# Optimization experiments

Hardware: AMD Instinct MI355X
Metric: run time of the kernel (lower is better)

The kernel has to match this reference:

```python
import jax, jax.numpy as jnp
import numpy as np

B, S, D, H = 4, 2048, 1024, 16
HD = D // H  # head_dim = 64


def setup_inputs() -> dict:
    key = jax.random.key(0)
    ks = jax.random.split(key, 5)
    hidden_states = jax.random.normal(ks[0], (B, S, D), dtype=jnp.float32)
    # GPT-2 Conv1D: out = x @ W + b, W shape [in, out]
    w_attn = jax.random.normal(ks[1], (D, 3 * D), dtype=jnp.float32) * 0.02
    b_attn = jnp.zeros((3 * D,), dtype=jnp.float32)
    w_proj = jax.random.normal(ks[2], (D, D), dtype=jnp.float32) * 0.02
    b_proj = jnp.zeros((D,), dtype=jnp.float32)
    return {"hidden_states": hidden_states, "w_attn": w_attn, "b_attn": b_attn,
            "w_proj": w_proj, "b_proj": b_proj}


def reference(hidden_states, w_attn, b_attn, w_proj, b_proj):
    b, s, d = hidden_states.shape
    qkv = hidden_states @ w_attn + b_attn                     # [B,S,3D]
    q, k, v = jnp.split(qkv, 3, axis=-1)
    # split heads -> [B,H,S,HD]
    def heads(x):
        return x.reshape(b, s, H, HD).transpose(0, 2, 1, 3)
    q, k, v = heads(q), heads(k), heads(v)
    # scaled dot product; GPT-2 divides by sqrt(head_dim)
    scores = jnp.einsum("bhqd,bhkd->bhqk", q, k) / jnp.sqrt(jnp.float32(HD))
    causal = jnp.tril(jnp.ones((s, s), dtype=bool))           # [S,S]
    neg = jnp.finfo(scores.dtype).min
    scores = jnp.where(causal[None, None, :, :], scores, neg)
    attn = jax.nn.softmax(scores, axis=-1)
    ctx = jnp.einsum("bhqk,bhkd->bhqd", attn, v)              # [B,H,S,HD]
    ctx = ctx.transpose(0, 2, 1, 3).reshape(b, s, d)          # merge heads
    return ctx @ w_proj + b_proj
```

## Files before the change

kernel.cpp:

```cpp
#include <hip/hip_runtime.h>
#include <hip/hip_bf16.h>

typedef __bf16 bf16;
typedef bf16 bf16x8 __attribute__((ext_vector_type(8)));
typedef bf16 bf16x4 __attribute__((ext_vector_type(4)));
typedef float f32x4 __attribute__((ext_vector_type(4)));
typedef float f32x16 __attribute__((ext_vector_type(16)));
typedef unsigned int uint2v __attribute__((ext_vector_type(2)));

#define MFMA16(a, b, c) __builtin_amdgcn_mfma_f32_16x16x32_bf16(a, b, c, 0, 0, 0)
#define MFMA32(a, b, c) __builtin_amdgcn_mfma_f32_32x32x16_bf16(a, b, c, 0, 0, 0)

constexpr int Bn = 4, Sn = 2048, Dn = 1024, Hn = 16, HDn = 64;
constexpr int Mn = Bn * Sn;

__device__ __forceinline__ bf16x8 cvt8(float4 a, float4 b) {
  bf16x8 v = {(bf16)a.x, (bf16)a.y, (bf16)a.z, (bf16)a.w,
              (bf16)b.x, (bf16)b.y, (bf16)b.z, (bf16)b.w};
  return v;
}

__device__ __forceinline__ void load_lds16(const bf16* g, bf16* l) {
  __builtin_amdgcn_global_load_lds(
      (const __attribute__((address_space(1))) void*)g,
      (__attribute__((address_space(3))) void*)l, 16, 0, 0);
}

__device__ __forceinline__ unsigned cvt_pk_bf16(float lo, float hi) {
  unsigned r;
  asm("v_cvt_pk_bf16_f32 %0, %1, %2" : "=v"(r) : "v"(lo), "v"(hi));
  return r;
}

__global__ __launch_bounds__(256) void k_cvt(const float* __restrict__ in,
                                             bf16* __restrict__ out) {
  int i = blockIdx.x * 256 + threadIdx.x;
  const float4* p = (const float4*)in + (size_t)i * 2;
  float4 a = p[0], b = p[1];
  *((bf16x8*)out + i) = cvt8(a, b);
}

__global__ __launch_bounds__(256) void k_transpose_cvt(const float* __restrict__ in,
                                                       bf16* __restrict__ out,
                                                       int K, int N) {
  __shared__ alignas(16) bf16 t[64][72];
  const int n0 = blockIdx.x * 64, k0 = blockIdx.y * 64;
  const int tid = threadIdx.x;
  {
    int row = tid >> 2;
    int c16 = (tid & 3) * 16;
    const float* src = in + (size_t)(k0 + row) * N + n0 + c16;
    float4 f0 = ((const float4*)src)[0];
    float4 f1 = ((const float4*)src)[1];
    float4 f2 = ((const float4*)src)[2];
    float4 f3 = ((const float4*)src)[3];
    *(bf16x8*)&t[row][c16] = cvt8(f0, f1);
    *(bf16x8*)&t[row][c16 + 8] = cvt8(f2, f3);
  }
  __syncthreads();
#pragma unroll
  for (int i = 0; i < 2; i++) {
    int c = tid + i * 256;
    int nrow = c >> 3, kcol8 = (c & 7) * 8;
    bf16x8 v;
#pragma unroll
    for (int j = 0; j < 8; j++) v[j] = t[kcol8 + j][nrow];
    *(bf16x8*)(out + (size_t)(n0 + nrow) * K + k0 + kcol8) = v;
  }
}


__global__ __launch_bounds__(256) void k_gemm_qkv(const bf16* __restrict__ A,
                                                  const bf16* __restrict__ BT,
                                                  const float* __restrict__ bias,
                                                  bf16* __restrict__ Qo,
                                                  bf16* __restrict__ Ko,
                                                  bf16* __restrict__ Vt) {
  __shared__ alignas(16) bf16 la[128 * 32];
  __shared__ alignas(16) bf16 lb[128 * 32];
  const int tid = threadIdx.x;
  const int w = tid >> 6, lane = tid & 63, l15 = lane & 15, quad = lane >> 4;
  const int wm = w >> 1, wn = w & 1;
  const int m0 = blockIdx.y * 128, n0 = blockIdx.x * 128;
  const int lrow = lane >> 2, lcol = (lane & 3) * 8;

  f32x4 acc[4][4];
#pragma unroll
  for (int i = 0; i < 4; i++)
#pragma unroll
    for (int j = 0; j < 4; j++) acc[i][j] = f32x4{0.f, 0.f, 0.f, 0.f};

  for (int k0 = 0; k0 < 1024; k0 += 32) {
    __syncthreads();
    load_lds16(A + (size_t)(m0 + w * 16 + lrow) * 1024 + k0 + lcol, &la[w * 512]);
    load_lds16(A + (size_t)(m0 + 64 + w * 16 + lrow) * 1024 + k0 + lcol, &la[(w + 4) * 512]);
    load_lds16(BT + (size_t)(n0 + w * 16 + lrow) * 1024 + k0 + lcol, &lb[w * 512]);
    load_lds16(BT + (size_t)(n0 + 64 + w * 16 + lrow) * 1024 + k0 + lcol, &lb[(w + 4) * 512]);
    __syncthreads();
    bf16x8 af[4], bfr[4];
#pragma unroll
    for (int i = 0; i < 4; i++)
      af[i] = *(const bf16x8*)&la[(wm * 64 + i * 16 + l15) * 32 + quad * 8];
#pragma unroll
    for (int j = 0; j < 4; j++)
      bfr[j] = *(const bf16x8*)&lb[(wn * 64 + j * 16 + l15) * 32 + quad * 8];
#pragma unroll
    for (int i = 0; i < 4; i++)
#pragma unroll
      for (int j = 0; j < 4; j++) acc[i][j] = MFMA16(af[i], bfr[j], acc[i][j]);
  }

#pragma unroll
  for (int j = 0; j < 4; j++) {
    int ng = n0 + wn * 64 + j * 16 + l15;
    float bs = bias[ng];
    int which = ng >> 10;
    int nloc = ng & 1023, hh = nloc >> 6, hd = nloc & 63;
#pragma unroll
    for (int i = 0; i < 4; i++) {
      int mg0 = m0 + wm * 64 + i * 16 + quad * 4;
      int bb = mg0 >> 11, ss = mg0 & 2047;
      if (which == 2) {
        bf16x4 v;
#pragma unroll
        for (int r = 0; r < 4; r++) v[r] = (bf16)(acc[i][j][r] + bs);
        *(bf16x4*)&Vt[((size_t)(bb * Hn + hh) * HDn + hd) * Sn + ss] = v;
      } else {
        bf16* dst = which ? Ko : Qo;
#pragma unroll
        for (int r = 0; r < 4; r++)
          dst[((size_t)(bb * Hn + hh) * Sn + ss + r) * HDn + hd] =
              (bf16)(acc[i][j][r] + bs);
      }
    }
  }
}

__global__ __launch_bounds__(256) void k_gemm_proj(const bf16* __restrict__ A,
                                                   const bf16* __restrict__ BT,
                                                   const float* __restrict__ bias,
                                                   float* __restrict__ out) {
  __shared__ alignas(16) bf16 la[128 * 32];
  __shared__ alignas(16) bf16 lb[128 * 32];
  const int tid = threadIdx.x;
  const int w = tid >> 6, lane = tid & 63, l15 = lane & 15, quad = lane >> 4;
  const int wm = w >> 1, wn = w & 1;
  const int m0 = blockIdx.y * 128, n0 = blockIdx.x * 128;
  const int lrow = lane >> 2, lcol = (lane & 3) * 8;

  f32x4 acc[4][4];
#pragma unroll
  for (int i = 0; i < 4; i++)
#pragma unroll
    for (int j = 0; j < 4; j++) acc[i][j] = f32x4{0.f, 0.f, 0.f, 0.f};

  for (int k0 = 0; k0 < 1024; k0 += 32) {
    __syncthreads();
    load_lds16(A + (size_t)(m0 + w * 16 + lrow) * 1024 + k0 + lcol, &la[w * 512]);
    load_lds16(A + (size_t)(m0 + 64 + w * 16 + lrow) * 1024 + k0 + lcol, &la[(w + 4) * 512]);
    load_lds16(BT + (size_t)(n0 + w * 16 + lrow) * 1024 + k0 + lcol, &lb[w * 512]);
    load_lds16(BT + (size_t)(n0 + 64 + w * 16 + lrow) * 1024 + k0 + lcol, &lb[(w + 4) * 512]);
    __syncthreads();
    bf16x8 af[4], bfr[4];
#pragma unroll
    for (int i = 0; i < 4; i++)
      af[i] = *(const bf16x8*)&la[(wm * 64 + i * 16 + l15) * 32 + quad * 8];
#pragma unroll
    for (int j = 0; j < 4; j++)
      bfr[j] = *(const bf16x8*)&lb[(wn * 64 + j * 16 + l15) * 32 + quad * 8];
#pragma unroll
    for (int i = 0; i < 4; i++)
#pragma unroll
      for (int j = 0; j < 4; j++) acc[i][j] = MFMA16(af[i], bfr[j], acc[i][j]);
  }

#pragma unroll
  for (int j = 0; j < 4; j++) {
    int ng = n0 + wn * 64 + j * 16 + l15;
    float bs = bias[ng];
#pragma unroll
    for (int i = 0; i < 4; i++) {
      int mg0 = m0 + wm * 64 + i * 16 + quad * 4;
#pragma unroll
      for (int r = 0; r < 4; r++)
        out[(size_t)(mg0 + r) * 1024 + ng] = acc[i][j][r] + bs;
    }
  }
}

__global__ __launch_bounds__(256) void k_attn(const bf16* __restrict__ Q,
                                              const bf16* __restrict__ Kv,
                                              const bf16* __restrict__ Vtg,
                                              bf16* __restrict__ ctx) {
  __shared__ alignas(16) bf16 kl[2][64 * 64];
  __shared__ alignas(16) bf16 vl[2][64 * 64];

  const int bh = blockIdx.x;
  const int qt = 15 - blockIdx.y;
  const int bb = bh >> 4, hh = bh & 15;
  const int tid = threadIdx.x;
  const int w = tid >> 6, lane = tid & 63, l31 = lane & 31, hi = lane >> 5;
  const size_t base = (size_t)bh * Sn * HDn;
  const int q0 = qt * 128 + w * 32;
  const int kend = qt * 128 + 128;

  const int r0 = tid >> 3, s0 = tid & 7;
  const int ksw = (s0 ^ (r0 & 7)) << 3;
  const bf16* Krow = Kv + base + (size_t)r0 * 64 + ksw;
  const bf16* Vrow0 = Vtg + ((size_t)bh * 64 + r0) * Sn + ksw;
  const bf16* Vrow1 = Vtg + ((size_t)bh * 64 + r0 + 32) * Sn + ksw;
  const int sw7 = l31 & 7;

  bf16x8 qf[4];
#pragma unroll
  for (int c = 0; c < 4; c++) {
    bf16x8 v = *(const bf16x8*)(Q + base + (size_t)(q0 + l31) * 64 + c * 16 + hi * 8);
#pragma unroll
    for (int e = 0; e < 8; e++) v[e] = (bf16)((float)v[e] * 0.125f);
    qf[c] = v;
  }

  f32x16 o0, o1;
#pragma unroll
  for (int e = 0; e < 16; e++) { o0[e] = 0.f; o1[e] = 0.f; }
  float dsum = 0.f;

  load_lds16(Krow, &kl[0][w * 512]);
  load_lds16(Krow + 32 * 64, &kl[0][2048 + w * 512]);
  load_lds16(Vrow0, &vl[0][w * 512]);
  load_lds16(Vrow1, &vl[0][2048 + w * 512]);

  int cur = 0;
  for (int kb = 0; kb < kend; kb += 64) {
    __syncthreads();
    if (kb + 64 < kend) {
      const int nk = kb + 64;
      load_lds16(Krow + (size_t)nk * 64, &kl[cur ^ 1][w * 512]);
      load_lds16(Krow + (size_t)(nk + 32) * 64, &kl[cur ^ 1][2048 + w * 512]);
      load_lds16(Vrow0 + nk, &vl[cur ^ 1][w * 512]);
      load_lds16(Vrow1 + nk, &vl[cur ^ 1][2048 + w * 512]);
    }
    if (kb <= q0 + 31) {
      const bf16* klc = kl[cur];
      const bf16* vlc = vl[cur];
#pragma unroll
      for (int sub = 0; sub < 2; sub++) {
        const int ks0 = kb + sub * 32;
        if (ks0 > q0 + 31) break;
        f32x16 st;
#pragma unroll
        for (int e = 0; e < 16; e++) st[e] = 0.f;
#pragma unroll
        for (int c = 0; c < 4; c++) {
          const int row = sub * 32 + l31;
          bf16x8 kf = *(const bf16x8*)&klc[row * 64 + (((2 * c + hi) ^ sw7) << 3)];
          st = MFMA32(kf, qf[c], st);
        }
        if (ks0 == q0) {
#pragma unroll
          for (int r = 0; r < 16; r++) {
            int krel = (r & 3) + 8 * (r >> 2) + 4 * hi;
            if (krel > l31) st[r] = -1e30f;
          }
        }
#pragma unroll
        for (int r = 0; r < 16; r++) {
          st[r] = __expf(st[r]);
          dsum += st[r];
        }
#pragma unroll
        for (int c2 = 0; c2 < 2; c2++) {
          unsigned wa0 = cvt_pk_bf16(st[8 * c2 + 0], st[8 * c2 + 1]);
          unsigned wa1 = cvt_pk_bf16(st[8 * c2 + 2], st[8 * c2 + 3]);
          unsigned wb0 = cvt_pk_bf16(st[8 * c2 + 4], st[8 * c2 + 5]);
          unsigned wb1 = cvt_pk_bf16(st[8 * c2 + 6], st[8 * c2 + 7]);
          unsigned pw0, pw1, pw2, pw3;
#if __has_builtin(__builtin_amdgcn_permlane32_swap)
          uint2v sw0 = __builtin_amdgcn_permlane32_swap(wa0, wb0, false, false);
          uint2v sw1 = __builtin_amdgcn_permlane32_swap(wa1, wb1, false, false);
          pw0 = sw0.x; pw1 = sw1.x; pw2 = sw0.y; pw3 = sw1.y;
#else
          unsigned xa0 = __shfl_xor((int)wa0, 32, 64), xb0 = __shfl_xor((int)wb0, 32, 64);
          unsigned xa1 = __shfl_xor((int)wa1, 32, 64), xb1 = __shfl_xor((int)wb1, 32, 64);
          pw0 = hi ? xb0 : wa0; pw1 = hi ? xb1 : wa1;
          pw2 = hi ? wb0 : xa0; pw3 = hi ? wb1 : xa1;
#endif
          union { unsigned u[4]; bf16x8 v; } pb;
          pb.u[0] = pw0; pb.u[1] = pw1; pb.u[2] = pw2; pb.u[3] = pw3;
          const int vs = sub * 4 + 2 * c2;
          bf16x8 vf0 = *(const bf16x8*)&vlc[l31 * 64 + (((vs + hi) ^ sw7) << 3)];
          o0 = MFMA32(vf0, pb.v, o0);
          bf16x8 vf1 = *(const bf16x8*)&vlc[(32 + l31) * 64 + (((vs + hi) ^ sw7) << 3)];
          o1 = MFMA32(vf1, pb.v, o1);
        }
      }
    }
    cur ^= 1;
  }

  float tot = dsum + __shfl_xor(dsum, 32, 64);
  float inv = 1.f / fmaxf(tot, 1e-20f);
  size_t ob = ((size_t)(bb * Sn + q0 + l31)) * Dn + hh * HDn + hi * 4;
#pragma unroll
  for (int g = 0; g < 4; g++) {
    bf16x4 v0, v1;
#pragma unroll
    for (int r = 0; r < 4; r++) {
      v0[r] = (bf16)(o0[4 * g + r] * inv);
      v1[r] = (bf16)(o1[4 * g + r] * inv);
    }
    *(bf16x4*)&ctx[ob + g * 8] = v0;
    *(bf16x4*)&ctx[ob + 32 + g * 8] = v1;
  }
}

extern "C" void kernel_launch(void* const* d_in, const int* in_sizes, int n_in,
                              void* d_out, int out_size, void* d_ws, size_t ws_size,
                              hipStream_t stream) {
  const float* hidden = (const float*)d_in[0];
  const float* w_attn = (const float*)d_in[1];
  const float* b_attn = (const float*)d_in[2];
  const float* w_proj = (const float*)d_in[3];
  const float* b_proj = (const float*)d_in[4];
  float* out = (float*)d_out;

  bf16* ws = (bf16*)d_ws;
  const size_t QKV_ELEMS = (size_t)Bn * Hn * Sn * HDn;
  bf16* Qb = ws;
  bf16* Kb = Qb + QKV_ELEMS;
  bf16* Vt = Kb + QKV_ELEMS;
  bf16* ctx = Vt + QKV_ELEMS;
  bf16* Xb = ctx;
  bf16* wattnT = ctx + (size_t)Mn * Dn;
  bf16* wprojT = wattnT + (size_t)Dn * 3 * Dn;

  k_cvt<<<4096, 256, 0, stream>>>(hidden, Xb);
  k_transpose_cvt<<<dim3(48, 16), 256, 0, stream>>>(w_attn, wattnT, 1024, 3072);
  k_transpose_cvt<<<dim3(16, 16), 256, 0, stream>>>(w_proj, wprojT, 1024, 1024);
  k_gemm_qkv<<<dim3(24, 64), 256, 0, stream>>>(Xb, wattnT, b_attn, Qb, Kb, Vt);
  k_attn<<<dim3(64, 16), 256, 0, stream>>>(Qb, Kb, Vt, ctx);
  k_gemm_proj<<<dim3(8, 64), 256, 0, stream>>>(ctx, wprojT, b_proj, out);
}
```

Baseline: 248.9 us.

## Rewrite QKV GEMM as 256x256 double-buffered pipelined tile with swizzled LDS

The QKV projection GEMM moves from 128x128 tiles with 256 threads and a synchronous K=32 loop to 256x256 tiles with 512 threads. It uses K=64 steps, double-buffered LDS filled by async global_load_lds, and an XOR swizzle against bank conflicts. Loads for later k-tiles are interleaved with MFMA phases using barriers, waitcnt and setprio, and a block-index swizzle improves L2 reuse. The aim is to hide memory latency and raise arithmetic intensity. The cost is 128KB of LDS per block and one block per CU, with fragile hand-tuned synchronisation.

```diff
diff --git a/kernel.cpp b/kernel.cpp
--- a/kernel.cpp
+++ b/kernel.cpp
@@ -69,56 +69,151 @@
   }
 }
 
-
-__global__ __launch_bounds__(256) void k_gemm_qkv(const bf16* __restrict__ A,
+__global__ __launch_bounds__(512) void k_gemm_qkv(const bf16* __restrict__ A,
                                                   const bf16* __restrict__ BT,
                                                   const float* __restrict__ bias,
                                                   bf16* __restrict__ Qo,
                                                   bf16* __restrict__ Ko,
                                                   bf16* __restrict__ Vt) {
-  __shared__ alignas(16) bf16 la[128 * 32];
-  __shared__ alignas(16) bf16 lb[128 * 32];
+  __shared__ alignas(16) bf16 lA[2][256 * 64];
+  __shared__ alignas(16) bf16 lB[2][256 * 64];
   const int tid = threadIdx.x;
   const int w = tid >> 6, lane = tid & 63, l15 = lane & 15, quad = lane >> 4;
-  const int wm = w >> 1, wn = w & 1;
-  const int m0 = blockIdx.y * 128, n0 = blockIdx.x * 128;
-  const int lrow = lane >> 2, lcol = (lane & 3) * 8;
-
-  f32x4 acc[4][4];
-#pragma unroll
-  for (int i = 0; i < 4; i++)
+  const int wm = w >> 2, wn = w & 3;
+  const int bid = blockIdx.x;
+  const int swz = (bid & 7) * 48 + (bid >> 3);
+  const int mblk = swz / 12, nblk = swz % 12;
+  const int m0 = mblk * 256, n0 = nblk * 256;
+  const int srow = tid >> 3;
+  const int scol = ((tid & 7) ^ ((tid >> 3) & 7)) * 8;
+  const int rsw = l15 & 7;
+
+  f32x4 acc[8][4];
+#pragma unroll
+  for (int i = 0; i < 8; i++)
 #pragma unroll
     for (int j = 0; j < 4; j++) acc[i][j] = f32x4{0.f, 0.f, 0.f, 0.f};
-
-  for (int k0 = 0; k0 < 1024; k0 += 32) {
-    __syncthreads();
-    load_lds16(A + (size_t)(m0 + w * 16 + lrow) * 1024 + k0 + lcol, &la[w * 512]);
-    load_lds16(A + (size_t)(m0 + 64 + w * 16 + lrow) * 1024 + k0 + lcol, &la[(w + 4) * 512]);
-    load_lds16(BT + (size_t)(n0 + w * 16 + lrow) * 1024 + k0 + lcol, &lb[w * 512]);
-    load_lds16(BT + (size_t)(n0 + 64 + w * 16 + lrow) * 1024 + k0 + lcol, &lb[(w + 4) * 512]);
-    __syncthreads();
-    bf16x8 af[4], bfr[4];
-#pragma unroll
-    for (int i = 0; i < 4; i++)
-      af[i] = *(const bf16x8*)&la[(wm * 64 + i * 16 + l15) * 32 + quad * 8];
-#pragma unroll
-    for (int j = 0; j < 4; j++)
-      bfr[j] = *(const bf16x8*)&lb[(wn * 64 + j * 16 + l15) * 32 + quad * 8];
-#pragma unroll
-    for (int i = 0; i < 4; i++)
-#pragma unroll
-      for (int j = 0; j < 4; j++) acc[i][j] = MFMA16(af[i], bfr[j], acc[i][j]);
-  }
-
+  bf16x8 Af[4][2], Bf[4][2];
+
+#define STAGE_A(bufi, tk, h)                                                      \
+  {                                                                               \
+    const bf16* s_ = A + (size_t)(m0 + (h) * 128 + srow) * 1024 + (tk) * 64 + scol; \
+    load_lds16(s_, &lA[bufi][(h) * 128 * 64] + w * 512);                          \
+    load_lds16(s_ + (size_t)64 * 1024, &lA[bufi][((h) * 128 + 64) * 64] + w * 512); \
+  }
+#define STAGE_B(bufi, tk, h)                                                      \
+  {                                                                               \
+    const bf16* s_ = BT + (size_t)(n0 + (h) * 128 + srow) * 1024 + (tk) * 64 + scol; \
+    load_lds16(s_, &lB[bufi][(h) * 128 * 64] + w * 512);                          \
+    load_lds16(s_ + (size_t)64 * 1024, &lB[bufi][((h) * 128 + 64) * 64] + w * 512); \
+  }
+
+  STAGE_B(0, 0, 0) STAGE_B(0, 0, 1)
+  STAGE_A(0, 0, 0) STAGE_A(0, 0, 1)
+  STAGE_B(1, 1, 0) STAGE_B(1, 1, 1)
+  asm volatile("s_waitcnt vmcnt(4)" ::: "memory");
+  __builtin_amdgcn_s_barrier();
+
+  auto tile_step = [&](int t, int buf) {
+    const bf16* la = &lA[buf][0];
+    const bf16* lb = &lB[buf][0];
+    const int tA = (t + 1) & 15, tB = (t + 2) & 15;
+#pragma unroll
+    for (int i = 0; i < 4; ++i)
+#pragma unroll
+      for (int ks = 0; ks < 2; ++ks)
+        Af[i][ks] = *(const bf16x8*)&la[(wm * 128 + i * 16 + l15) * 64 +
+                                        (((ks * 4 + quad) ^ rsw) << 3)];
+#pragma unroll
+    for (int j = 0; j < 2; ++j)
+#pragma unroll
+      for (int ks = 0; ks < 2; ++ks)
+        Bf[j][ks] = *(const bf16x8*)&lb[(wn * 64 + j * 16 + l15) * 64 +
+                                        (((ks * 4 + quad) ^ rsw) << 3)];
+    STAGE_A(buf ^ 1, tA, 0)
+    __builtin_amdgcn_s_barrier();
+    asm volatile("s_waitcnt lgkmcnt(0)" ::: "memory");
+    __builtin_amdgcn_sched_barrier(0);
+    __builtin_amdgcn_s_setprio(1);
+#pragma unroll
+    for (int i = 0; i < 4; ++i)
+#pragma unroll
+      for (int j = 0; j < 2; ++j)
+#pragma unroll
+        for (int ks = 0; ks < 2; ++ks)
+          acc[i][j] = MFMA16(Af[i][ks], Bf[j][ks], acc[i][j]);
+    __builtin_amdgcn_s_setprio(0);
+    __builtin_amdgcn_s_barrier();
+#pragma unroll
+    for (int j = 2; j < 4; ++j)
+#pragma unroll
+      for (int ks = 0; ks < 2; ++ks)
+        Bf[j][ks] = *(const bf16x8*)&lb[(wn * 64 + j * 16 + l15) * 64 +
+                                        (((ks * 4 + quad) ^ rsw) << 3)];
+    STAGE_A(buf ^ 1, tA, 1)
+    __builtin_amdgcn_s_barrier();
+    asm volatile("s_waitcnt lgkmcnt(0)" ::: "memory");
+    __builtin_amdgcn_sched_barrier(0);
+    __builtin_amdgcn_s_setprio(1);
+#pragma unroll
+    for (int i = 0; i < 4; ++i)
+#pragma unroll
+      for (int j = 2; j < 4; ++j)
+#pragma unroll
+        for (int ks = 0; ks < 2; ++ks)
+          acc[i][j] = MFMA16(Af[i][ks], Bf[j][ks], acc[i][j]);
+    __builtin_amdgcn_s_setprio(0);
+    __builtin_amdgcn_s_barrier();
+#pragma unroll
+    for (int i = 0; i < 4; ++i)
+#pragma unroll
+      for (int ks = 0; ks < 2; ++ks)
+        Af[i][ks] = *(const bf16x8*)&la[(wm * 128 + (4 + i) * 16 + l15) * 64 +
+                                        (((ks * 4 + quad) ^ rsw) << 3)];
+    STAGE_B(buf, tB, 0)
+    __builtin_amdgcn_s_barrier();
+    asm volatile("s_waitcnt lgkmcnt(0)" ::: "memory");
+    __builtin_amdgcn_sched_barrier(0);
+    __builtin_amdgcn_s_setprio(1);
+#pragma unroll
+    for (int i = 0; i < 4; ++i)
+#pragma unroll
+      for (int j = 2; j < 4; ++j)
+#pragma unroll
+        for (int ks = 0; ks < 2; ++ks)
+          acc[4 + i][j] = MFMA16(Af[i][ks], Bf[j][ks], acc[4 + i][j]);
+    __builtin_amdgcn_s_setprio(0);
+    __builtin_amdgcn_s_barrier();
+    STAGE_B(buf, tB, 1)
+    __builtin_amdgcn_s_barrier();
+    __builtin_amdgcn_s_setprio(1);
+#pragma unroll
+    for (int i = 0; i < 4; ++i)
+#pragma unroll
+      for (int j = 0; j < 2; ++j)
+#pragma unroll
+        for (int ks = 0; ks < 2; ++ks)
+          acc[4 + i][j] = MFMA16(Af[i][ks], Bf[j][ks], acc[4 + i][j]);
+    __builtin_amdgcn_s_setprio(0);
+    asm volatile("s_waitcnt vmcnt(4)" ::: "memory");
+    __builtin_amdgcn_s_barrier();
+  };
+
+  for (int th = 0; th < 8; ++th) {
+    tile_step(2 * th, 0);
+    tile_step(2 * th + 1, 1);
+  }
+  asm volatile("s_waitcnt vmcnt(0)" ::: "memory");
+
+  const int which = n0 >> 10;
 #pragma unroll
   for (int j = 0; j < 4; j++) {
     int ng = n0 + wn * 64 + j * 16 + l15;
     float bs = bias[ng];
-    int which = ng >> 10;
     int nloc = ng & 1023, hh = nloc >> 6, hd = nloc & 63;
 #pragma unroll
-    for (int i = 0; i < 4; i++) {
-      int mg0 = m0 + wm * 64 + i * 16 + quad * 4;
+    for (int i = 0; i < 8; i++) {
+      int mg0 = m0 + wm * 128 + i * 16 + quad * 4;
       int bb = mg0 >> 11, ss = mg0 & 2047;
       if (which == 2) {
         bf16x4 v;
@@ -134,6 +229,8 @@
       }
     }
   }
+#undef STAGE_A
+#undef STAGE_B
 }
 
 __global__ __launch_bounds__(256) void k_gemm_proj(const bf16* __restrict__ A,
@@ -337,7 +434,7 @@
   k_cvt<<<4096, 256, 0, stream>>>(hidden, Xb);
   k_transpose_cvt<<<dim3(48, 16), 256, 0, stream>>>(w_attn, wattnT, 1024, 3072);
   k_transpose_cvt<<<dim3(16, 16), 256, 0, stream>>>(w_proj, wprojT, 1024, 1024);
-  k_gemm_qkv<<<dim3(24, 64), 256, 0, stream>>>(Xb, wattnT, b_attn, Qb, Kb, Vt);
+  k_gemm_qkv<<<dim3(384), 512, 0, stream>>>(Xb, wattnT, b_attn, Qb, Kb, Vt);
   k_attn<<<dim3(64, 16), 256, 0, stream>>>(Qb, Kb, Vt, ctx);
   k_gemm_proj<<<dim3(8, 64), 256, 0, stream>>>(ctx, wprojT, b_proj, out);
 }
```

Measured after the change: 255.9 us. 2.8% more time.

## Triple-buffer attention K/V loads and merge prep kernels into one launch

Applied to the files above, without the earlier changes.

The attention kernel moves from double to triple buffering of K/V tiles in LDS. It prefetches two tiles ahead and replaces __syncthreads with an explicit vmcnt wait plus s_barrier, so global-to-LDS loads overlap more of the compute. Separately, the three input conversion and transpose kernels are merged into one launch, with each block choosing its job from its block index, which saves two launches. The cost is 16KB more LDS per attention block, which may lower occupancy, and the hand-tuned vmcnt counts depend on how many loads each stage issues.

```diff
diff --git a/kernel.cpp b/kernel.cpp
--- a/kernel.cpp
+++ b/kernel.cpp
@@ -32,20 +32,34 @@
   return r;
 }
 
-__global__ __launch_bounds__(256) void k_cvt(const float* __restrict__ in,
-                                             bf16* __restrict__ out) {
-  int i = blockIdx.x * 256 + threadIdx.x;
-  const float4* p = (const float4*)in + (size_t)i * 2;
-  float4 a = p[0], b = p[1];
-  *((bf16x8*)out + i) = cvt8(a, b);
-}
-
-__global__ __launch_bounds__(256) void k_transpose_cvt(const float* __restrict__ in,
-                                                       bf16* __restrict__ out,
-                                                       int K, int N) {
+__global__ __launch_bounds__(256) void k_prep(const float* __restrict__ hidden,
+                                              const float* __restrict__ w_attn,
+                                              const float* __restrict__ w_proj,
+                                              bf16* __restrict__ Xb,
+                                              bf16* __restrict__ wattnT,
+                                              bf16* __restrict__ wprojT) {
   __shared__ alignas(16) bf16 t[64][72];
-  const int n0 = blockIdx.x * 64, k0 = blockIdx.y * 64;
+  const int bx = blockIdx.x;
   const int tid = threadIdx.x;
+  if (bx < 4096) {
+    int i = bx * 256 + tid;
+    const float4* p = (const float4*)hidden + (size_t)i * 2;
+    float4 a = p[0], b = p[1];
+    *((bf16x8*)Xb + i) = cvt8(a, b);
+    return;
+  }
+  const float* in;
+  bf16* out;
+  int K = 1024, N, n0, k0;
+  if (bx < 4864) {
+    int idx = bx - 4096;
+    in = w_attn; out = wattnT; N = 3072;
+    n0 = (idx % 48) * 64; k0 = (idx / 48) * 64;
+  } else {
+    int idx = bx - 4864;
+    in = w_proj; out = wprojT; N = 1024;
+    n0 = (idx % 16) * 64; k0 = (idx / 16) * 64;
+  }
   {
     int row = tid >> 2;
     int c16 = (tid & 3) * 16;
@@ -192,8 +206,8 @@
                                               const bf16* __restrict__ Kv,
                                               const bf16* __restrict__ Vtg,
                                               bf16* __restrict__ ctx) {
-  __shared__ alignas(16) bf16 kl[2][64 * 64];
-  __shared__ alignas(16) bf16 vl[2][64 * 64];
+  __shared__ alignas(16) bf16 kl[3][64 * 64];
+  __shared__ alignas(16) bf16 vl[3][64 * 64];
 
   const int bh = blockIdx.x;
   const int qt = 15 - blockIdx.y;
@@ -202,7 +216,7 @@
   const int w = tid >> 6, lane = tid & 63, l31 = lane & 31, hi = lane >> 5;
   const size_t base = (size_t)bh * Sn * HDn;
   const int q0 = qt * 128 + w * 32;
-  const int kend = qt * 128 + 128;
+  const int nt = 2 * qt + 2;
 
   const int r0 = tid >> 3, s0 = tid & 7;
   const int ksw = (s0 ^ (r0 & 7)) << 3;
@@ -225,24 +239,28 @@
   for (int e = 0; e < 16; e++) { o0[e] = 0.f; o1[e] = 0.f; }
   float dsum = 0.f;
 
-  load_lds16(Krow, &kl[0][w * 512]);
-  load_lds16(Krow + 32 * 64, &kl[0][2048 + w * 512]);
-  load_lds16(Vrow0, &vl[0][w * 512]);
-  load_lds16(Vrow1, &vl[0][2048 + w * 512]);
-
-  int cur = 0;
-  for (int kb = 0; kb < kend; kb += 64) {
-    __syncthreads();
-    if (kb + 64 < kend) {
-      const int nk = kb + 64;
-      load_lds16(Krow + (size_t)nk * 64, &kl[cur ^ 1][w * 512]);
-      load_lds16(Krow + (size_t)(nk + 32) * 64, &kl[cur ^ 1][2048 + w * 512]);
-      load_lds16(Vrow0 + nk, &vl[cur ^ 1][w * 512]);
-      load_lds16(Vrow1 + nk, &vl[cur ^ 1][2048 + w * 512]);
-    }
+#define STAGE(t_, bf_)                                                  \
+  {                                                                     \
+    const int kb_ = (t_) * 64;                                          \
+    load_lds16(Krow + (size_t)kb_ * 64, &kl[bf_][w * 512]);             \
+    load_lds16(Krow + (size_t)(kb_ + 32) * 64, &kl[bf_][2048 + w * 512]); \
+    load_lds16(Vrow0 + kb_, &vl[bf_][w * 512]);                         \
+    load_lds16(Vrow1 + kb_, &vl[bf_][2048 + w * 512]);                  \
+  }
+
+  STAGE(0, 0)
+  STAGE(1, 1)
+
+  int cb = 0, sb = 2;
+  for (int t = 0; t < nt; ++t) {
+    if (t == nt - 1) asm volatile("s_waitcnt vmcnt(0)" ::: "memory");
+    else             asm volatile("s_waitcnt vmcnt(4)" ::: "memory");
+    __builtin_amdgcn_s_barrier();
+    if (t + 2 < nt) STAGE(t + 2, sb)
+    const int kb = t * 64;
     if (kb <= q0 + 31) {
-      const bf16* klc = kl[cur];
-      const bf16* vlc = vl[cur];
+      const bf16* klc = kl[cb];
+      const bf16* vlc = vl[cb];
 #pragma unroll
       for (int sub = 0; sub < 2; sub++) {
         const int ks0 = kb + sub * 32;
@@ -295,8 +313,10 @@
         }
       }
     }
-    cur ^= 1;
-  }
+    cb = (cb == 2) ? 0 : cb + 1;
+    sb = (sb == 2) ? 0 : sb + 1;
+  }
+#undef STAGE
 
   float tot = dsum + __shfl_xor(dsum, 32, 64);
   float inv = 1.f / fmaxf(tot, 1e-20f);
@@ -334,9 +354,7 @@
   bf16* wattnT = ctx + (size_t)Mn * Dn;
   bf16* wprojT = wattnT + (size_t)Dn * 3 * Dn;
 
-  k_cvt<<<4096, 256, 0, stream>>>(hidden, Xb);
-  k_transpose_cvt<<<dim3(48, 16), 256, 0, stream>>>(w_attn, wattnT, 1024, 3072);
-  k_transpose_cvt<<<dim3(16, 16), 256, 0, stream>>>(w_proj, wprojT, 1024, 1024);
+  k_prep<<<5120, 256, 0, stream>>>(hidden, w_attn, w_proj, Xb, wattnT, wprojT);
   k_gemm_qkv<<<dim3(24, 64), 256, 0, stream>>>(Xb, wattnT, b_attn, Qb, Kb, Vt);
   k_attn<<<dim3(64, 16), 256, 0, stream>>>(Qb, Kb, Vt, ctx);
   k_gemm_proj<<<dim3(8, 64), 256, 0, stream>>>(ctx, wprojT, b_proj, out);
```

Measured after the change: 241.3 us. 1.03x faster.
